# Kernel tuning notes

Measured on AMD Instinct MI355X. Metric: run time of the kernel, lower is better.

Reference implementation:

```python
import jax, jax.numpy as jnp
import numpy as np


def setup_inputs() -> dict:
    key = jax.random.key(0)
    k1, k2, k3, k4, k5 = jax.random.split(key, 5)
    B, S, D, U = 64, 2048, 512, 512
    he = lambda k, shape: jax.random.normal(k, shape, dtype=jnp.float32) * jnp.sqrt(2.0 / shape[0])
    return {
        "query": jax.random.normal(k1, (B, D), dtype=jnp.float32),
        "values": jax.random.normal(k2, (B, S, D), dtype=jnp.float32),
        "W1": he(k3, (D, U)),
        "W2": he(k4, (D, U)),
        "V1": he(k5, (U, 1)),
    }


def reference(query, values, W1, W2, V1):
    # query: (B, D), values: (B, S, D)
    Q = query @ W1                       # (B, U)
    V = jnp.einsum("bsd,du->bsu", values, W2)  # (B, S, U)
    add = jnp.tanh(Q[:, None, :] + V)    # (B, S, U)
    score = jnp.einsum("bsu,uo->bso", add, V1)  # (B, S, 1)
    attn = jax.nn.softmax(score, axis=1)         # (B, S, 1)
    context = jnp.sum(attn * values, axis=1)     # (B, D)
    return context
```

## Files before the change

kernel.cpp:

```cpp
#include <hip/hip_runtime.h>


typedef __attribute__((ext_vector_type(8))) short bf16x8;
typedef __attribute__((ext_vector_type(4))) float f32x4;

#if __has_builtin(__builtin_amdgcn_exp2f)
__device__ __forceinline__ float fast_exp2(float x) { return __builtin_amdgcn_exp2f(x); }
#else
__device__ __forceinline__ float fast_exp2(float x) { return exp2f(x); }
#endif
#if __has_builtin(__builtin_amdgcn_rcpf)
__device__ __forceinline__ float fast_rcp(float x) { return __builtin_amdgcn_rcpf(x); }
#else
__device__ __forceinline__ float fast_rcp(float x) { return 1.0f / x; }
#endif

__device__ __forceinline__ unsigned short f2bf(float f) {
  unsigned int u = __float_as_uint(f);
  u += 0x7fffu + ((u >> 16) & 1u);
  return (unsigned short)(u >> 16);
}

__global__ void qk(const float* __restrict__ query, const float* __restrict__ W1,
                   float* __restrict__ Q) {
  __shared__ float qrow[512];
  const int b = blockIdx.x, half = blockIdx.y, t = threadIdx.x;
  qrow[t] = query[b * 512 + t];
  qrow[t + 256] = query[b * 512 + t + 256];
  __syncthreads();
  const int u = half * 256 + t;
  float acc = 0.f;
#pragma unroll 8
  for (int k = 0; k < 512; ++k) acc += qrow[k] * W1[(size_t)k * 512 + u];
  Q[b * 512 + u] = acc;
}

__global__ void wt_k(const float* __restrict__ W2, unsigned short* __restrict__ Wtf) {
  const int gid = blockIdx.x * 256 + threadIdx.x;
  const int lane = gid & 63;
  const int g = gid >> 6;
  const int ks = g & 15, ntile = g >> 4;
  const int l15 = lane & 15, quad = lane >> 4;
  const int n = ntile * 16 + l15;
  const int k0 = ks * 32 + quad * 8;
  unsigned int p[4];
#pragma unroll
  for (int jj = 0; jj < 4; ++jj) {
    const float a = W2[(size_t)(k0 + 2 * jj) * 512 + n];
    const float b = W2[(size_t)(k0 + 2 * jj + 1) * 512 + n];
    p[jj] = (unsigned int)f2bf(a) | ((unsigned int)f2bf(b) << 16);
  }
  *(uint4*)&Wtf[(size_t)gid * 8] = make_uint4(p[0], p[1], p[2], p[3]);
}

__global__ __launch_bounds__(512, 4) void scorectx_k(
    const float* __restrict__ values, const unsigned short* __restrict__ Wtf,
    const float* __restrict__ Q, const float* __restrict__ V1,
    float* __restrict__ Pstat, float* __restrict__ Pctx) {
  __shared__ __align__(16) unsigned short Ab[64 * 512];
  __shared__ float sAcc[64];
  __shared__ float wLDS[64];

  const int t = threadIdx.x;
  const int lane = t & 63;
  const int w = t >> 6;
  const int quad = lane >> 4;
  const int l15 = lane & 15;
  const int blk = blockIdx.x;
  const int m0 = blk * 64;
  const int b = m0 >> 11;

  if (t < 64) sAcc[t] = 0.0f;

  const float* Ag = values + (size_t)m0 * 512;
#pragma unroll
  for (int i = 0; i < 8; ++i) {
    const int c = i * 512 + t;
    const int m = c >> 6;
    const int kc = c & 63;
    const float4* src = (const float4*)(Ag + (size_t)m * 512 + kc * 8);
    const float4 x = src[0], y = src[1];
    const unsigned int p0 = (unsigned int)f2bf(x.x) | ((unsigned int)f2bf(x.y) << 16);
    const unsigned int p1 = (unsigned int)f2bf(x.z) | ((unsigned int)f2bf(x.w) << 16);
    const unsigned int p2 = (unsigned int)f2bf(y.x) | ((unsigned int)f2bf(y.y) << 16);
    const unsigned int p3 = (unsigned int)f2bf(y.z) | ((unsigned int)f2bf(y.w) << 16);
    *(uint4*)&Ab[m * 512 + ((kc ^ (m & 7)) * 8)] = make_uint4(p0, p1, p2, p3);
  }
  __syncthreads();

  f32x4 acc[4][4];
#pragma unroll
  for (int mt = 0; mt < 4; ++mt)
#pragma unroll
    for (int nt = 0; nt < 4; ++nt) acc[mt][nt] = (f32x4){0.f, 0.f, 0.f, 0.f};

  const unsigned short* Bg = Wtf + (size_t)lane * 8;
  const int sw = l15 & 7;

#pragma unroll
  for (int ks = 0; ks < 16; ++ks) {
    bf16x8 bfr[4], af[4];
#pragma unroll
    for (int nt = 0; nt < 4; ++nt)
      bfr[nt] = *(const bf16x8*)(Bg + (size_t)((w * 4 + nt) * 16 + ks) * 512);
#pragma unroll
    for (int mt = 0; mt < 4; ++mt) {
      const int m = mt * 16 + l15;
      af[mt] = *(const bf16x8*)&Ab[m * 512 + (((ks * 4 + quad) ^ sw) * 8)];
    }
#pragma unroll
    for (int mt = 0; mt < 4; ++mt)
#pragma unroll
      for (int nt = 0; nt < 4; ++nt)
        acc[mt][nt] = __builtin_amdgcn_mfma_f32_16x16x32_bf16(af[mt], bfr[nt],
                                                              acc[mt][nt], 0, 0, 0);
  }

  float part[4][4];
#pragma unroll
  for (int mt = 0; mt < 4; ++mt)
#pragma unroll
    for (int r = 0; r < 4; ++r) part[mt][r] = 0.f;

#pragma unroll
  for (int nt = 0; nt < 4; ++nt) {
    const int n = w * 64 + nt * 16 + l15;
    const float qv = Q[b * 512 + n];
    const float v1 = V1[n];
#pragma unroll
    for (int mt = 0; mt < 4; ++mt)
#pragma unroll
      for (int r = 0; r < 4; ++r) {
        const float x = acc[mt][nt][r] + qv;
        const float e = fast_exp2(x * 2.8853900817779268f);
        const float th = 1.0f - 2.0f * fast_rcp(e + 1.0f);
        part[mt][r] += th * v1;
      }
  }
#pragma unroll
  for (int mt = 0; mt < 4; ++mt)
#pragma unroll
    for (int r = 0; r < 4; ++r) {
      float v = part[mt][r];
      v += __shfl_xor(v, 1);
      v += __shfl_xor(v, 2);
      v += __shfl_xor(v, 4);
      v += __shfl_xor(v, 8);
      if (l15 == 0) atomicAdd(&sAcc[mt * 16 + quad * 4 + r], v);
    }
  __syncthreads();

  const float L2E = 1.4426950408889634f;
  if (t < 64) {
    const float v = sAcc[t];
    float m = v;
#pragma unroll
    for (int o = 1; o < 64; o <<= 1) m = fmaxf(m, __shfl_xor(m, o));
    const float wv = fast_exp2((v - m) * L2E);
    float dsum = wv;
#pragma unroll
    for (int o = 1; o < 64; o <<= 1) dsum += __shfl_xor(dsum, o);
    wLDS[t] = wv;
    if (t == 0) {
      Pstat[2 * blk] = m;
      Pstat[2 * blk + 1] = dsum;
    }
  }
  __syncthreads();

  const float* vrow = values + (size_t)m0 * 512 + t;
  float cacc = 0.f;
#pragma unroll 8
  for (int r = 0; r < 64; ++r) cacc += wLDS[r] * vrow[(size_t)r * 512];
  Pctx[(size_t)blk * 512 + t] = cacc;
}

__global__ __launch_bounds__(512) void comb_k(const float* __restrict__ Pstat,
                                              const float* __restrict__ Pctx,
                                              float* __restrict__ out) {
  __shared__ float aL[32];
  __shared__ float Dsh;
  const int b = blockIdx.x, t = threadIdx.x;
  const float L2E = 1.4426950408889634f;
  if (t < 32) {
    const float2 st = ((const float2*)Pstat)[b * 32 + t];
    float m = st.x;
#pragma unroll
    for (int o = 1; o < 32; o <<= 1) m = fmaxf(m, __shfl_xor(m, o));
    const float a = fast_exp2((st.x - m) * L2E);
    float D = a * st.y;
#pragma unroll
    for (int o = 1; o < 32; o <<= 1) D += __shfl_xor(D, o);
    aL[t] = a;
    if (t == 0) Dsh = D;
  }
  __syncthreads();
  const float* pc = Pctx + (size_t)b * 32 * 512 + t;
  float acc = 0.f;
#pragma unroll
  for (int i = 0; i < 32; ++i) acc += aL[i] * pc[(size_t)i * 512];
  out[b * 512 + t] = acc / Dsh;
}

extern "C" void kernel_launch(void* const* d_in, const int* in_sizes, int n_in,
                              void* d_out, int out_size, void* d_ws, size_t ws_size,
                              hipStream_t stream) {
  const float* query = (const float*)d_in[0];
  const float* values = (const float*)d_in[1];
  const float* W1 = (const float*)d_in[2];
  const float* W2 = (const float*)d_in[3];
  const float* V1 = (const float*)d_in[4];
  float* out = (float*)d_out;

  char* ws = (char*)d_ws;
  float* Qp = (float*)ws;
  unsigned short* Wtp = (unsigned short*)(ws + 131072);
  float* Pstat = (float*)(ws + 131072 + 524288);
  float* Pctx = (float*)(ws + 131072 + 524288 + 16384);

  qk<<<dim3(64, 2), 256, 0, stream>>>(query, W1, Qp);
  wt_k<<<128, 256, 0, stream>>>(W2, Wtp);
  scorectx_k<<<2048, 512, 0, stream>>>(values, Wtp, Qp, V1, Pstat, Pctx);
  comb_k<<<64, 512, 0, stream>>>(Pstat, Pctx, out);
}
```

Before: 477.3 us.

## Split score GEMM into two N-halves with register double-buffered operand prefetch

The per-wave 64x64 MFMA tile becomes two sequential passes of 64x32, so the accumulator live set is halved. Inside each pass the B fragments for the next k-step come from global memory and the A fragments from LDS, both fetched before the current step's MFMAs run, to hide load latency. The launch-bounds occupancy hint drops from 4 to 2 blocks, which gives the compiler more registers. The trade-offs are lower occupancy, and a second tanh/reduction/atomic epilogue that re-reads A from LDS twice.

```diff
diff --git a/kernel.cpp b/kernel.cpp
--- a/kernel.cpp
+++ b/kernel.cpp
@@ -53,7 +53,7 @@
   *(uint4*)&Wtf[(size_t)gid * 8] = make_uint4(p[0], p[1], p[2], p[3]);
 }
 
-__global__ __launch_bounds__(512, 4) void scorectx_k(
+__global__ __launch_bounds__(512, 2) void scorectx_k(
     const float* __restrict__ values, const unsigned short* __restrict__ Wtf,
     const float* __restrict__ Q, const float* __restrict__ V1,
     float* __restrict__ Pstat, float* __restrict__ Pctx) {
@@ -88,66 +88,86 @@
   }
   __syncthreads();
 
-  f32x4 acc[4][4];
-#pragma unroll
-  for (int mt = 0; mt < 4; ++mt)
-#pragma unroll
-    for (int nt = 0; nt < 4; ++nt) acc[mt][nt] = (f32x4){0.f, 0.f, 0.f, 0.f};
-
-  const unsigned short* Bg = Wtf + (size_t)lane * 8;
   const int sw = l15 & 7;
-
-#pragma unroll
-  for (int ks = 0; ks < 16; ++ks) {
-    bf16x8 bfr[4], af[4];
-#pragma unroll
-    for (int nt = 0; nt < 4; ++nt)
-      bfr[nt] = *(const bf16x8*)(Bg + (size_t)((w * 4 + nt) * 16 + ks) * 512);
+  const unsigned short* Blane = Wtf + (size_t)lane * 8;
+
+#pragma unroll
+  for (int nh = 0; nh < 2; ++nh) {
+    const int t0 = nh * 16 + w * 2;
+    const unsigned short* B0 = Blane + (size_t)(t0 * 16) * 512;
+    const unsigned short* B1 = Blane + (size_t)((t0 + 1) * 16) * 512;
+
+    f32x4 acc[4][2];
 #pragma unroll
     for (int mt = 0; mt < 4; ++mt) {
-      const int m = mt * 16 + l15;
-      af[mt] = *(const bf16x8*)&Ab[m * 512 + (((ks * 4 + quad) ^ sw) * 8)];
-    }
+      acc[mt][0] = (f32x4){0.f, 0.f, 0.f, 0.f};
+      acc[mt][1] = (f32x4){0.f, 0.f, 0.f, 0.f};
+    }
+
+    bf16x8 bc0 = *(const bf16x8*)B0;
+    bf16x8 bc1 = *(const bf16x8*)B1;
+    bf16x8 ac[4];
 #pragma unroll
     for (int mt = 0; mt < 4; ++mt)
-#pragma unroll
-      for (int nt = 0; nt < 4; ++nt)
-        acc[mt][nt] = __builtin_amdgcn_mfma_f32_16x16x32_bf16(af[mt], bfr[nt],
-                                                              acc[mt][nt], 0, 0, 0);
-  }
-
-  float part[4][4];
-#pragma unroll
-  for (int mt = 0; mt < 4; ++mt)
-#pragma unroll
-    for (int r = 0; r < 4; ++r) part[mt][r] = 0.f;
-
-#pragma unroll
-  for (int nt = 0; nt < 4; ++nt) {
-    const int n = w * 64 + nt * 16 + l15;
-    const float qv = Q[b * 512 + n];
-    const float v1 = V1[n];
+      ac[mt] = *(const bf16x8*)&Ab[(mt * 16 + l15) * 512 + ((quad ^ sw) * 8)];
+
+#pragma unroll
+    for (int ks = 0; ks < 16; ++ks) {
+      bf16x8 bn0, bn1, an[4];
+      if (ks < 15) {
+        bn0 = *(const bf16x8*)(B0 + (size_t)(ks + 1) * 512);
+        bn1 = *(const bf16x8*)(B1 + (size_t)(ks + 1) * 512);
+#pragma unroll
+        for (int mt = 0; mt < 4; ++mt)
+          an[mt] = *(const bf16x8*)&Ab[(mt * 16 + l15) * 512 +
+                                       ((((ks + 1) * 4 + quad) ^ sw) * 8)];
+      }
+#pragma unroll
+      for (int mt = 0; mt < 4; ++mt) {
+        acc[mt][0] = __builtin_amdgcn_mfma_f32_16x16x32_bf16(ac[mt], bc0, acc[mt][0], 0, 0, 0);
+        acc[mt][1] = __builtin_amdgcn_mfma_f32_16x16x32_bf16(ac[mt], bc1, acc[mt][1], 0, 0, 0);
+      }
+      if (ks < 15) {
+        bc0 = bn0;
+        bc1 = bn1;
+#pragma unroll
+        for (int mt = 0; mt < 4; ++mt) ac[mt] = an[mt];
+      }
+    }
+
+    float part[4][4];
 #pragma unroll
     for (int mt = 0; mt < 4; ++mt)
 #pragma unroll
+      for (int r = 0; r < 4; ++r) part[mt][r] = 0.f;
+
+#pragma unroll
+    for (int nt = 0; nt < 2; ++nt) {
+      const int n = (t0 + nt) * 16 + l15;
+      const float qv = Q[b * 512 + n];
+      const float v1 = V1[n];
+#pragma unroll
+      for (int mt = 0; mt < 4; ++mt)
+#pragma unroll
+        for (int r = 0; r < 4; ++r) {
+          const float x = acc[mt][nt][r] + qv;
+          const float e = fast_exp2(x * 2.8853900817779268f);
+          const float th = 1.0f - 2.0f * fast_rcp(e + 1.0f);
+          part[mt][r] += th * v1;
+        }
+    }
+#pragma unroll
+    for (int mt = 0; mt < 4; ++mt)
+#pragma unroll
       for (int r = 0; r < 4; ++r) {
-        const float x = acc[mt][nt][r] + qv;
-        const float e = fast_exp2(x * 2.8853900817779268f);
-        const float th = 1.0f - 2.0f * fast_rcp(e + 1.0f);
-        part[mt][r] += th * v1;
-      }
-  }
-#pragma unroll
-  for (int mt = 0; mt < 4; ++mt)
-#pragma unroll
-    for (int r = 0; r < 4; ++r) {
-      float v = part[mt][r];
-      v += __shfl_xor(v, 1);
-      v += __shfl_xor(v, 2);
-      v += __shfl_xor(v, 4);
-      v += __shfl_xor(v, 8);
-      if (l15 == 0) atomicAdd(&sAcc[mt * 16 + quad * 4 + r], v);
-    }
+        float v = part[mt][r];
+        v += __shfl_xor(v, 1);
+        v += __shfl_xor(v, 2);
+        v += __shfl_xor(v, 4);
+        v += __shfl_xor(v, 8);
+        if (l15 == 0) atomicAdd(&sAcc[mt * 16 + quad * 4 + r], v);
+      }
+  }
   __syncthreads();
 
   const float L2E = 1.4426950408889634f;
```

Result: slower. 492.8 us (+3.3%).
